# Kernel tuning notes

Hardware: AMD Instinct MI355X
Metric: run time of the kernel (lower is better)

The kernel has to match this reference:

```python
import jax, jax.numpy as jnp
import numpy as np

B, S, H = 8, 1024, 1024
NH, HD = 16, 64
EPS = 1e-12


def _p(w, g):
    # make_p_layer: w + gamma * clamp(w, min=0)
    return w + g * jnp.clip(w, 0.0, None)


def _pproc(x, W, b, g):
    # z = layer(x); zp = player(x); return zp * (z/zp).detach()  (value == z)
    z = x @ W.T + b
    zp = x @ _p(W, g).T + _p(b, g)
    return zp * jax.lax.stop_gradient(z / zp)


def _ln_nowb_detach(x):
    # 'nowb' LayerNorm (no weight/bias), mean and std detached (LNargsDetach)
    m = jax.lax.stop_gradient(jnp.mean(x, axis=-1, keepdims=True))
    v = jax.lax.stop_gradient(jnp.var(x, axis=-1, keepdims=True))
    return (x - m) / jnp.sqrt(v + EPS)


def setup_inputs() -> dict:
    key = jax.random.key(0)
    ks = jax.random.split(key, 10)
    lin = lambda k: (jax.random.normal(k, (H, H), jnp.float32) * 0.02)
    vec = lambda k: (jax.random.normal(k, (H,), jnp.float32) * 0.02)
    return {
        "hidden_states": jax.random.normal(ks[0], (B, S, H), jnp.float32),
        "Wq": lin(ks[1]), "bq": vec(ks[2]),
        "Wk": lin(ks[3]), "bk": vec(ks[4]),
        "Wv": lin(ks[5]), "bv": vec(ks[6]),
        "Wo": lin(ks[7]), "bo": vec(ks[8]),
        "gamma_AH": jnp.float32(0.1),
        "gamma_LN": jnp.float32(0.1),
    }


def reference(hidden_states, Wq, bq, Wk, bk, Wv, bv, Wo, bo, gamma_AH, gamma_LN):
    g = gamma_AH
    # dual-pass Q/K/V (pproc: value == plain linear, grads via perturbed layer)
    q = _pproc(hidden_states, Wq, bq, g)   # [B,S,H]
    k = _pproc(hidden_states, Wk, bk, g)
    v = _pproc(hidden_states, Wv, bv, g)
    split = lambda x: x.reshape(B, S, NH, HD).transpose(0, 2, 1, 3)  # [B,NH,S,HD]
    qt, kt, vt = split(q), split(k), split(v)
    # NOTE: original code does NOT scale by 1/sqrt(head_dim)
    scores = jnp.einsum('bhqd,bhkd->bhqk', qt, kt)
    attn = jax.nn.softmax(scores, axis=-1)
    probs = (1.0 - g) * jax.lax.stop_gradient(attn) + g * attn
    ctx = jnp.einsum('bhqk,bhkd->bhqd', probs, vt)
    ctx = ctx.transpose(0, 2, 1, 3).reshape(B, S, H)  # [B,S,H]
    # BertSelfOutput.pforward: perturbed dense (gamma_LN) + residual + detached LN
    h = ctx @ _p(Wo, gamma_LN).T + _p(bo, gamma_LN)
    out = _ln_nowb_detach(h + hidden_states)
    return out, probs
```

## Files before the change

kernel.cpp:

```cpp
#include <hip/hip_runtime.h>

typedef short short8 __attribute__((ext_vector_type(8)));
typedef float floatx4 __attribute__((ext_vector_type(4)));
typedef unsigned short ushort8v __attribute__((ext_vector_type(8)));

#define B_ 8
#define S_ 1024
#define H_ 1024
#define NH_ 16
#define HD_ 64

__device__ __forceinline__ unsigned short f2bf(float f) {
  unsigned u = __float_as_uint(f);
  u += 0x7fffu + ((u >> 16) & 1u);
  return (unsigned short)(u >> 16);
}

__device__ __forceinline__ floatx4 mfma16(short8 a, short8 b, floatx4 c) {
  return __builtin_amdgcn_mfma_f32_16x16x32_bf16(a, b, c, 0, 0, 0);
}

__global__ void __launch_bounds__(256) cvt_kernel(const float* __restrict__ src,
                                                  unsigned short* __restrict__ dst,
                                                  const float* __restrict__ gamma,
                                                  int n) {
  int i = (blockIdx.x * 256 + threadIdx.x) * 4;
  if (i >= n) return;
  float g = gamma ? gamma[0] : 0.0f;
  float4 v = *(const float4*)(src + i);
  ushort4 o;
  o.x = f2bf(v.x + g * fmaxf(v.x, 0.f));
  o.y = f2bf(v.y + g * fmaxf(v.y, 0.f));
  o.z = f2bf(v.z + g * fmaxf(v.z, 0.f));
  o.w = f2bf(v.w + g * fmaxf(v.w, 0.f));
  *(ushort4*)(dst + i) = o;
}

__device__ __forceinline__ void gemm_mainloop(const unsigned short* __restrict__ Ag,
                                              const unsigned short* __restrict__ Bg,
                                              int K,
                                              unsigned short* As, unsigned short* Bs,
                                              floatx4 acc[4][4]) {
  const int tid = threadIdx.x;
  const int l = tid & 63, w = tid >> 6;
  const int l15 = l & 15, l4 = l >> 4;
  const int wm = (w & 1) << 6, wn = (w >> 1) << 6;
  const int r0 = tid >> 2;
  const int c0 = (tid & 3) << 3;
  for (int k0 = 0; k0 < K; k0 += 32) {
    __syncthreads();
    *(uint4*)&As[r0 * 32 + c0]        = *(const uint4*)&Ag[(size_t)r0 * K + k0 + c0];
    *(uint4*)&As[(r0 + 64) * 32 + c0] = *(const uint4*)&Ag[(size_t)(r0 + 64) * K + k0 + c0];
    *(uint4*)&Bs[r0 * 32 + c0]        = *(const uint4*)&Bg[(size_t)r0 * K + k0 + c0];
    *(uint4*)&Bs[(r0 + 64) * 32 + c0] = *(const uint4*)&Bg[(size_t)(r0 + 64) * K + k0 + c0];
    __syncthreads();
    short8 a[4], bb[4];
#pragma unroll
    for (int i = 0; i < 4; ++i)
      a[i] = *(const short8*)&As[(wm + i * 16 + l15) * 32 + l4 * 8];
#pragma unroll
    for (int j = 0; j < 4; ++j)
      bb[j] = *(const short8*)&Bs[(wn + j * 16 + l15) * 32 + l4 * 8];
#pragma unroll
    for (int i = 0; i < 4; ++i)
#pragma unroll
      for (int j = 0; j < 4; ++j)
        acc[i][j] = mfma16(a[i], bb[j], acc[i][j]);
  }
}

__global__ void __launch_bounds__(256) gemm_qkv(
    const unsigned short* __restrict__ xb,
    const unsigned short* __restrict__ wq, const unsigned short* __restrict__ wk,
    const unsigned short* __restrict__ wv,
    const float* __restrict__ bq, const float* __restrict__ bk, const float* __restrict__ bv,
    unsigned short* __restrict__ oq, unsigned short* __restrict__ ok,
    unsigned short* __restrict__ ov) {
  __shared__ unsigned short As[128 * 32];
  __shared__ unsigned short Bs[128 * 32];
  const int z = blockIdx.z;
  const unsigned short* W = (z == 0) ? wq : (z == 1) ? wk : wv;
  const float* bias        = (z == 0) ? bq : (z == 1) ? bk : bv;
  unsigned short* O        = (z == 0) ? oq : (z == 1) ? ok : ov;
  const int nBase = blockIdx.x * 128, mBase = blockIdx.y * 128;
  floatx4 acc[4][4];
  const floatx4 fz = {0.f, 0.f, 0.f, 0.f};
#pragma unroll
  for (int i = 0; i < 4; ++i)
#pragma unroll
    for (int j = 0; j < 4; ++j) acc[i][j] = fz;
  gemm_mainloop(xb + (size_t)mBase * H_, W + (size_t)nBase * H_, H_, As, Bs, acc);
  const int l = threadIdx.x & 63, w = threadIdx.x >> 6;
  const int l15 = l & 15, l4 = l >> 4;
  const int wm = (w & 1) << 6, wn = (w >> 1) << 6;
#pragma unroll
  for (int i = 0; i < 4; ++i) {
    int row = mBase + wm + i * 16 + l4 * 4;
#pragma unroll
    for (int j = 0; j < 4; ++j) {
      int col = nBase + wn + j * 16 + l15;
      float bcol = bias[col];
#pragma unroll
      for (int r = 0; r < 4; ++r)
        O[(size_t)(row + r) * H_ + col] = f2bf(acc[i][j][r] + bcol);
    }
  }
}

__global__ void __launch_bounds__(256) transpose_v(const unsigned short* __restrict__ vb,
                                                   unsigned short* __restrict__ vt) {
  const int st = blockIdx.x, h = blockIdx.y, b = blockIdx.z;
  __shared__ unsigned short t[64 * 72];
  const int tid = threadIdx.x;
  const unsigned short* src = vb + (size_t)(b * S_ + st * 64) * H_ + h * HD_;
  for (int c = tid; c < 512; c += 256) {
    int i = c >> 3, dg = (c & 7) << 3;
    *(uint4*)&t[i * 72 + dg] = *(const uint4*)&src[(size_t)i * H_ + dg];
  }
  __syncthreads();
  unsigned short* dst = vt + ((size_t)(b * NH_ + h) * HD_) * S_ + st * 64;
  for (int c = tid; c < 512; c += 256) {
    int d = c >> 3, ig = (c & 7) << 3;
    ushort8v v;
#pragma unroll
    for (int ii = 0; ii < 8; ++ii) v[ii] = t[(ig + ii) * 72 + d];
    *(ushort8v*)&dst[(size_t)d * S_ + ig] = v;
  }
}

__global__ void __launch_bounds__(256) attn_kernel(
    const unsigned short* __restrict__ qg_, const unsigned short* __restrict__ kg_,
    const unsigned short* __restrict__ vtg_,
    float* __restrict__ probs, unsigned short* __restrict__ ctxb) {
  const int qt = blockIdx.x, h = blockIdx.y, b = blockIdx.z;
  __shared__ unsigned short Qs[64 * 64];
  __shared__ unsigned short Ks[128 * 64];
  __shared__ unsigned short Vts[64 * 128];
  __shared__ unsigned short Ps[64 * 128];
  const int tid = threadIdx.x;
  const int l = tid & 63, w = tid >> 6;
  const int l15 = l & 15, l4 = l >> 4;

  const unsigned short* qg = qg_ + ((size_t)(b * S_) + qt * 64) * H_ + h * HD_;
  const unsigned short* kg = kg_ + (size_t)(b * S_) * H_ + h * HD_;
  const unsigned short* vg = vtg_ + ((size_t)(b * NH_ + h) * HD_) * S_;

  for (int c = tid; c < 512; c += 256) {
    int row = c >> 3, cg = (c & 7) << 3;
    *(uint4*)&Qs[row * 64 + cg] = *(const uint4*)&qg[(size_t)row * H_ + cg];
  }
  __syncthreads();
  short8 aq0 = *(const short8*)&Qs[(w * 16 + l15) * 64 + l4 * 8];
  short8 aq1 = *(const short8*)&Qs[(w * 16 + l15) * 64 + 32 + l4 * 8];

  float esum[4] = {0.f, 0.f, 0.f, 0.f};
  for (int kt = 0; kt < 8; ++kt) {
    __syncthreads();
    for (int c = tid; c < 1024; c += 256) {
      int row = c >> 3, cg = (c & 7) << 3;
      *(uint4*)&Ks[row * 64 + cg] = *(const uint4*)&kg[(size_t)(kt * 128 + row) * H_ + cg];
    }
    __syncthreads();
#pragma unroll
    for (int j = 0; j < 8; ++j) {
      short8 b0 = *(const short8*)&Ks[(j * 16 + l15) * 64 + l4 * 8];
      short8 b1 = *(const short8*)&Ks[(j * 16 + l15) * 64 + 32 + l4 * 8];
      floatx4 s = {0.f, 0.f, 0.f, 0.f};
      s = mfma16(aq0, b0, s);
      s = mfma16(aq1, b1, s);
#pragma unroll
      for (int r = 0; r < 4; ++r) esum[r] += __expf(s[r]);
    }
  }
#pragma unroll
  for (int m = 1; m < 16; m <<= 1)
#pragma unroll
    for (int r = 0; r < 4; ++r) esum[r] += __shfl_xor(esum[r], m, 64);
  float rinv[4];
#pragma unroll
  for (int r = 0; r < 4; ++r) rinv[r] = 1.0f / esum[r];

  const floatx4 fz = {0.f, 0.f, 0.f, 0.f};
  floatx4 cacc[4];
#pragma unroll
  for (int dt = 0; dt < 4; ++dt) cacc[dt] = fz;
  const int qrow_base = qt * 64 + w * 16 + l4 * 4;
  for (int kt = 0; kt < 8; ++kt) {
    __syncthreads();
    for (int c = tid; c < 1024; c += 256) {
      int row = c >> 3, cg = (c & 7) << 3;
      *(uint4*)&Ks[row * 64 + cg] = *(const uint4*)&kg[(size_t)(kt * 128 + row) * H_ + cg];
    }
    for (int c = tid; c < 1024; c += 256) {
      int row = c >> 4, cg = (c & 15) << 3;
      *(uint4*)&Vts[row * 128 + cg] = *(const uint4*)&vg[(size_t)row * S_ + kt * 128 + cg];
    }
    __syncthreads();
#pragma unroll
    for (int j = 0; j < 8; ++j) {
      short8 b0 = *(const short8*)&Ks[(j * 16 + l15) * 64 + l4 * 8];
      short8 b1 = *(const short8*)&Ks[(j * 16 + l15) * 64 + 32 + l4 * 8];
      floatx4 s = {0.f, 0.f, 0.f, 0.f};
      s = mfma16(aq0, b0, s);
      s = mfma16(aq1, b1, s);
      float* pp = probs + ((size_t)((b * NH_ + h) * S_) + qrow_base) * S_ + kt * 128 + j * 16 + l15;
#pragma unroll
      for (int r = 0; r < 4; ++r) {
        float p = __expf(s[r]) * rinv[r];
        pp[(size_t)r * S_] = p;
        Ps[(w * 16 + l4 * 4 + r) * 128 + j * 16 + l15] = f2bf(p);
      }
    }
    __syncthreads();
    short8 ap[4];
#pragma unroll
    for (int ks = 0; ks < 4; ++ks)
      ap[ks] = *(const short8*)&Ps[(w * 16 + l15) * 128 + ks * 32 + l4 * 8];
#pragma unroll
    for (int dt = 0; dt < 4; ++dt)
#pragma unroll
      for (int ks = 0; ks < 4; ++ks) {
        short8 bv = *(const short8*)&Vts[(dt * 16 + l15) * 128 + ks * 32 + l4 * 8];
        cacc[dt] = mfma16(ap[ks], bv, cacc[dt]);
      }
  }
  const int rowg = b * S_ + qt * 64 + w * 16 + l4 * 4;
#pragma unroll
  for (int dt = 0; dt < 4; ++dt)
#pragma unroll
    for (int r = 0; r < 4; ++r)
      ctxb[(size_t)(rowg + r) * H_ + h * HD_ + dt * 16 + l15] = f2bf(cacc[dt][r]);
}

__global__ void __launch_bounds__(256) gemm_out(
    const unsigned short* __restrict__ ctxb, const unsigned short* __restrict__ wob,
    const float* __restrict__ bo, const float* __restrict__ gln,
    const float* __restrict__ xres, float* __restrict__ hres) {
  __shared__ unsigned short As[128 * 32];
  __shared__ unsigned short Bs[128 * 32];
  const int nBase = blockIdx.x * 128, mBase = blockIdx.y * 128;
  floatx4 acc[4][4];
  const floatx4 fz = {0.f, 0.f, 0.f, 0.f};
#pragma unroll
  for (int i = 0; i < 4; ++i)
#pragma unroll
    for (int j = 0; j < 4; ++j) acc[i][j] = fz;
  gemm_mainloop(ctxb + (size_t)mBase * H_, wob + (size_t)nBase * H_, H_, As, Bs, acc);
  const float g = gln[0];
  const int l = threadIdx.x & 63, w = threadIdx.x >> 6;
  const int l15 = l & 15, l4 = l >> 4;
  const int wm = (w & 1) << 6, wn = (w >> 1) << 6;
#pragma unroll
  for (int i = 0; i < 4; ++i) {
    int row = mBase + wm + i * 16 + l4 * 4;
#pragma unroll
    for (int j = 0; j < 4; ++j) {
      int col = nBase + wn + j * 16 + l15;
      float pb = bo[col];
      pb += g * fmaxf(pb, 0.f);
#pragma unroll
      for (int r = 0; r < 4; ++r)
        hres[(size_t)(row + r) * H_ + col] =
            acc[i][j][r] + pb + xres[(size_t)(row + r) * H_ + col];
    }
  }
}

__global__ void __launch_bounds__(256) ln_kernel(const float* __restrict__ hres,
                                                 float* __restrict__ out) {
  const int row = blockIdx.x;
  const int tid = threadIdx.x;
  const float* xr = hres + (size_t)row * H_;
  float4 v = *(const float4*)&xr[tid * 4];
  float s = v.x + v.y + v.z + v.w;
  float q = v.x * v.x + v.y * v.y + v.z * v.z + v.w * v.w;
#pragma unroll
  for (int m = 1; m < 64; m <<= 1) {
    s += __shfl_xor(s, m, 64);
    q += __shfl_xor(q, m, 64);
  }
  __shared__ float sh[8];
  const int w = tid >> 6, l = tid & 63;
  if (l == 0) { sh[w] = s; sh[4 + w] = q; }
  __syncthreads();
  s = sh[0] + sh[1] + sh[2] + sh[3];
  q = sh[4] + sh[5] + sh[6] + sh[7];
  float mean = s * (1.f / 1024.f);
  float var = q * (1.f / 1024.f) - mean * mean;
  float inv = rsqrtf(var + 1e-12f);
  float4 o;
  o.x = (v.x - mean) * inv;
  o.y = (v.y - mean) * inv;
  o.z = (v.z - mean) * inv;
  o.w = (v.w - mean) * inv;
  *(float4*)&out[(size_t)row * H_ + tid * 4] = o;
}

extern "C" void kernel_launch(void* const* d_in, const int* in_sizes, int n_in,
                              void* d_out, int out_size, void* d_ws, size_t ws_size,
                              hipStream_t stream) {
  const float* x   = (const float*)d_in[0];
  const float* Wq  = (const float*)d_in[1];
  const float* bq  = (const float*)d_in[2];
  const float* Wk  = (const float*)d_in[3];
  const float* bk  = (const float*)d_in[4];
  const float* Wv  = (const float*)d_in[5];
  const float* bv  = (const float*)d_in[6];
  const float* Wo  = (const float*)d_in[7];
  const float* bo  = (const float*)d_in[8];
  const float* gLN = (const float*)d_in[10];

  float* out   = (float*)d_out;
  float* probs = out + (size_t)B_ * S_ * H_;

  unsigned short* xb  = (unsigned short*)d_ws;
  unsigned short* wqb = xb + 8388608;
  unsigned short* wkb = wqb + 1048576;
  unsigned short* wvb = wkb + 1048576;
  unsigned short* wob = wvb + 1048576;
  unsigned short* qb  = wob + 1048576;
  unsigned short* kb  = qb + 8388608;
  unsigned short* vb  = kb + 8388608;
  unsigned short* vt  = vb + 8388608;
  unsigned short* ctxb = xb;
  float* hres = (float*)qb;

  cvt_kernel<<<8192, 256, 0, stream>>>(x, xb, nullptr, 8388608);
  cvt_kernel<<<1024, 256, 0, stream>>>(Wq, wqb, nullptr, 1048576);
  cvt_kernel<<<1024, 256, 0, stream>>>(Wk, wkb, nullptr, 1048576);
  cvt_kernel<<<1024, 256, 0, stream>>>(Wv, wvb, nullptr, 1048576);
  cvt_kernel<<<1024, 256, 0, stream>>>(Wo, wob, gLN, 1048576);

  gemm_qkv<<<dim3(8, 64, 3), 256, 0, stream>>>(xb, wqb, wkb, wvb, bq, bk, bv, qb, kb, vb);
  transpose_v<<<dim3(16, 16, 8), 256, 0, stream>>>(vb, vt);
  attn_kernel<<<dim3(16, 16, 8), 256, 0, stream>>>(qb, kb, vt, probs, ctxb);
  gemm_out<<<dim3(8, 64, 1), 256, 0, stream>>>(ctxb, wob, bo, gLN, x, hres);
  ln_kernel<<<8192, 256, 0, stream>>>(hres, out);
}
```

Before: 971.9 us.

## Use direct global-to-LDS loads with XOR-swizzled LDS layouts and merge weight converts

Replaces register-staged global->LDS copies in the GEMM mainloop and attention kernel with global_load_lds 16-byte direct loads. In attention, K, V^T and P tiles use an XOR swizzle so MFMA operand reads avoid LDS bank conflicts. The four weight conversion launches are merged into one kernel. This aims to cut VGPR traffic, bank conflicts and launch overhead, but it relies on the lane-to-address mapping that global_load_lds requires and adds index arithmetic.

```diff
diff --git a/kernel.cpp b/kernel.cpp
--- a/kernel.cpp
+++ b/kernel.cpp
@@ -20,13 +20,32 @@
   return __builtin_amdgcn_mfma_f32_16x16x32_bf16(a, b, c, 0, 0, 0);
 }
 
-__global__ void __launch_bounds__(256) cvt_kernel(const float* __restrict__ src,
-                                                  unsigned short* __restrict__ dst,
-                                                  const float* __restrict__ gamma,
-                                                  int n) {
+__device__ __forceinline__ void gload16(const void* g, void* lds) {
+  __builtin_amdgcn_global_load_lds(
+      (const __attribute__((address_space(1))) unsigned int*)g,
+      (__attribute__((address_space(3))) unsigned int*)lds, 16, 0, 0);
+}
+
+__global__ void __launch_bounds__(256) cvt_x(const float* __restrict__ src,
+                                             unsigned short* __restrict__ dst) {
   int i = (blockIdx.x * 256 + threadIdx.x) * 4;
-  if (i >= n) return;
-  float g = gamma ? gamma[0] : 0.0f;
+  float4 v = *(const float4*)(src + i);
+  ushort4 o;
+  o.x = f2bf(v.x); o.y = f2bf(v.y); o.z = f2bf(v.z); o.w = f2bf(v.w);
+  *(ushort4*)(dst + i) = o;
+}
+
+__global__ void __launch_bounds__(256) cvt_w(
+    const float* __restrict__ W0, const float* __restrict__ W1,
+    const float* __restrict__ W2, const float* __restrict__ W3,
+    unsigned short* __restrict__ o0, unsigned short* __restrict__ o1,
+    unsigned short* __restrict__ o2, unsigned short* __restrict__ o3,
+    const float* __restrict__ gLN) {
+  const int which = blockIdx.y;
+  const float* src = (which == 0) ? W0 : (which == 1) ? W1 : (which == 2) ? W2 : W3;
+  unsigned short* dst = (which == 0) ? o0 : (which == 1) ? o1 : (which == 2) ? o2 : o3;
+  const float g = (which == 3) ? gLN[0] : 0.0f;
+  int i = (blockIdx.x * 256 + threadIdx.x) * 4;
   float4 v = *(const float4*)(src + i);
   ushort4 o;
   o.x = f2bf(v.x + g * fmaxf(v.x, 0.f));
@@ -45,14 +64,14 @@
   const int l = tid & 63, w = tid >> 6;
   const int l15 = l & 15, l4 = l >> 4;
   const int wm = (w & 1) << 6, wn = (w >> 1) << 6;
-  const int r0 = tid >> 2;
-  const int c0 = (tid & 3) << 3;
+  const int srow = w * 32 + (l >> 2);
+  const int scol = (l & 3) << 3;
   for (int k0 = 0; k0 < K; k0 += 32) {
     __syncthreads();
-    *(uint4*)&As[r0 * 32 + c0]        = *(const uint4*)&Ag[(size_t)r0 * K + k0 + c0];
-    *(uint4*)&As[(r0 + 64) * 32 + c0] = *(const uint4*)&Ag[(size_t)(r0 + 64) * K + k0 + c0];
-    *(uint4*)&Bs[r0 * 32 + c0]        = *(const uint4*)&Bg[(size_t)r0 * K + k0 + c0];
-    *(uint4*)&Bs[(r0 + 64) * 32 + c0] = *(const uint4*)&Bg[(size_t)(r0 + 64) * K + k0 + c0];
+    gload16(&Ag[(size_t)srow * K + k0 + scol],        &As[srow * 32 + scol]);
+    gload16(&Ag[(size_t)(srow + 16) * K + k0 + scol], &As[(srow + 16) * 32 + scol]);
+    gload16(&Bg[(size_t)srow * K + k0 + scol],        &Bs[srow * 32 + scol]);
+    gload16(&Bg[(size_t)(srow + 16) * K + k0 + scol], &Bs[(srow + 16) * 32 + scol]);
     __syncthreads();
     short8 a[4], bb[4];
 #pragma unroll
@@ -76,8 +95,8 @@
     const float* __restrict__ bq, const float* __restrict__ bk, const float* __restrict__ bv,
     unsigned short* __restrict__ oq, unsigned short* __restrict__ ok,
     unsigned short* __restrict__ ov) {
-  __shared__ unsigned short As[128 * 32];
-  __shared__ unsigned short Bs[128 * 32];
+  __shared__ __align__(16) unsigned short As[128 * 32];
+  __shared__ __align__(16) unsigned short Bs[128 * 32];
   const int z = blockIdx.z;
   const unsigned short* W = (z == 0) ? wq : (z == 1) ? wk : wv;
   const float* bias        = (z == 0) ? bq : (z == 1) ? bk : bv;
@@ -110,7 +129,7 @@
 __global__ void __launch_bounds__(256) transpose_v(const unsigned short* __restrict__ vb,
                                                    unsigned short* __restrict__ vt) {
   const int st = blockIdx.x, h = blockIdx.y, b = blockIdx.z;
-  __shared__ unsigned short t[64 * 72];
+  __shared__ __align__(16) unsigned short t[64 * 72];
   const int tid = threadIdx.x;
   const unsigned short* src = vb + (size_t)(b * S_ + st * 64) * H_ + h * HD_;
   for (int c = tid; c < 512; c += 256) {
@@ -133,21 +152,25 @@
     const unsigned short* __restrict__ vtg_,
     float* __restrict__ probs, unsigned short* __restrict__ ctxb) {
   const int qt = blockIdx.x, h = blockIdx.y, b = blockIdx.z;
-  __shared__ unsigned short Qs[64 * 64];
-  __shared__ unsigned short Ks[128 * 64];
-  __shared__ unsigned short Vts[64 * 128];
-  __shared__ unsigned short Ps[64 * 128];
+  __shared__ __align__(16) unsigned short Qs[64 * 64];
+  __shared__ __align__(16) unsigned short Ks[128 * 64];
+  __shared__ __align__(16) unsigned short Vts[64 * 128];
+  __shared__ __align__(16) unsigned short Ps[64 * 128];
   const int tid = threadIdx.x;
   const int l = tid & 63, w = tid >> 6;
   const int l15 = l & 15, l4 = l >> 4;
+  const int l7 = l & 7, lr8 = l >> 3;
 
   const unsigned short* qg = qg_ + ((size_t)(b * S_) + qt * 64) * H_ + h * HD_;
   const unsigned short* kg = kg_ + (size_t)(b * S_) * H_ + h * HD_;
   const unsigned short* vg = vtg_ + ((size_t)(b * NH_ + h) * HD_) * S_;
 
-  for (int c = tid; c < 512; c += 256) {
-    int row = c >> 3, cg = (c & 7) << 3;
-    *(uint4*)&Qs[row * 64 + cg] = *(const uint4*)&qg[(size_t)row * H_ + cg];
+  const int kcol = (l7 ^ lr8) << 3;
+
+#pragma unroll
+  for (int c = 0; c < 2; ++c) {
+    int row = w * 16 + c * 8 + lr8;
+    gload16(&qg[(size_t)row * H_ + (l7 << 3)], &Qs[row * 64 + (l7 << 3)]);
   }
   __syncthreads();
   short8 aq0 = *(const short8*)&Qs[(w * 16 + l15) * 64 + l4 * 8];
@@ -156,15 +179,17 @@
   float esum[4] = {0.f, 0.f, 0.f, 0.f};
   for (int kt = 0; kt < 8; ++kt) {
     __syncthreads();
-    for (int c = tid; c < 1024; c += 256) {
-      int row = c >> 3, cg = (c & 7) << 3;
-      *(uint4*)&Ks[row * 64 + cg] = *(const uint4*)&kg[(size_t)(kt * 128 + row) * H_ + cg];
+#pragma unroll
+    for (int c = 0; c < 4; ++c) {
+      int row = w * 32 + c * 8 + lr8;
+      gload16(&kg[(size_t)(kt * 128 + row) * H_ + kcol], &Ks[row * 64 + (l7 << 3)]);
     }
     __syncthreads();
 #pragma unroll
     for (int j = 0; j < 8; ++j) {
-      short8 b0 = *(const short8*)&Ks[(j * 16 + l15) * 64 + l4 * 8];
-      short8 b1 = *(const short8*)&Ks[(j * 16 + l15) * 64 + 32 + l4 * 8];
+      int rr = l15 & 7;
+      short8 b0 = *(const short8*)&Ks[(j * 16 + l15) * 64 + ((l4 ^ rr) << 3)];
+      short8 b1 = *(const short8*)&Ks[(j * 16 + l15) * 64 + (((4 + l4) ^ rr) << 3)];
       floatx4 s = {0.f, 0.f, 0.f, 0.f};
       s = mfma16(aq0, b0, s);
       s = mfma16(aq1, b1, s);
@@ -187,19 +212,23 @@
   const int qrow_base = qt * 64 + w * 16 + l4 * 4;
   for (int kt = 0; kt < 8; ++kt) {
     __syncthreads();
-    for (int c = tid; c < 1024; c += 256) {
-      int row = c >> 3, cg = (c & 7) << 3;
-      *(uint4*)&Ks[row * 64 + cg] = *(const uint4*)&kg[(size_t)(kt * 128 + row) * H_ + cg];
-    }
-    for (int c = tid; c < 1024; c += 256) {
-      int row = c >> 4, cg = (c & 15) << 3;
-      *(uint4*)&Vts[row * 128 + cg] = *(const uint4*)&vg[(size_t)row * S_ + kt * 128 + cg];
+#pragma unroll
+    for (int c = 0; c < 4; ++c) {
+      int row = w * 32 + c * 8 + lr8;
+      gload16(&kg[(size_t)(kt * 128 + row) * H_ + kcol], &Ks[row * 64 + (l7 << 3)]);
+    }
+#pragma unroll
+    for (int c = 0; c < 4; ++c) {
+      int row = w * 16 + c * 4 + l4;
+      int scol = (l15 ^ (c * 4 + l4)) << 3;
+      gload16(&vg[(size_t)row * S_ + kt * 128 + scol], &Vts[row * 128 + (l15 << 3)]);
     }
     __syncthreads();
 #pragma unroll
     for (int j = 0; j < 8; ++j) {
-      short8 b0 = *(const short8*)&Ks[(j * 16 + l15) * 64 + l4 * 8];
-      short8 b1 = *(const short8*)&Ks[(j * 16 + l15) * 64 + 32 + l4 * 8];
+      int rr = l15 & 7;
+      short8 b0 = *(const short8*)&Ks[(j * 16 + l15) * 64 + ((l4 ^ rr) << 3)];
+      short8 b1 = *(const short8*)&Ks[(j * 16 + l15) * 64 + (((4 + l4) ^ rr) << 3)];
       floatx4 s = {0.f, 0.f, 0.f, 0.f};
       s = mfma16(aq0, b0, s);
       s = mfma16(aq1, b1, s);
@@ -208,19 +237,21 @@
       for (int r = 0; r < 4; ++r) {
         float p = __expf(s[r]) * rinv[r];
         pp[(size_t)r * S_] = p;
-        Ps[(w * 16 + l4 * 4 + r) * 128 + j * 16 + l15] = f2bf(p);
+        int prow = w * 16 + l4 * 4 + r;
+        int pslot = (j * 2 + (l15 >> 3)) ^ (l4 * 4 + r);
+        Ps[prow * 128 + (pslot << 3) + (l15 & 7)] = f2bf(p);
       }
     }
     __syncthreads();
     short8 ap[4];
 #pragma unroll
     for (int ks = 0; ks < 4; ++ks)
-      ap[ks] = *(const short8*)&Ps[(w * 16 + l15) * 128 + ks * 32 + l4 * 8];
+      ap[ks] = *(const short8*)&Ps[(w * 16 + l15) * 128 + (((ks * 4 + l4) ^ l15) << 3)];
 #pragma unroll
     for (int dt = 0; dt < 4; ++dt)
 #pragma unroll
       for (int ks = 0; ks < 4; ++ks) {
-        short8 bv = *(const short8*)&Vts[(dt * 16 + l15) * 128 + ks * 32 + l4 * 8];
+        short8 bv = *(const short8*)&Vts[(dt * 16 + l15) * 128 + (((ks * 4 + l4) ^ l15) << 3)];
         cacc[dt] = mfma16(ap[ks], bv, cacc[dt]);
       }
   }
@@ -236,8 +267,8 @@
     const unsigned short* __restrict__ ctxb, const unsigned short* __restrict__ wob,
     const float* __restrict__ bo, const float* __restrict__ gln,
     const float* __restrict__ xres, float* __restrict__ hres) {
-  __shared__ unsigned short As[128 * 32];
-  __shared__ unsigned short Bs[128 * 32];
+  __shared__ __align__(16) unsigned short As[128 * 32];
+  __shared__ __align__(16) unsigned short Bs[128 * 32];
   const int nBase = blockIdx.x * 128, mBase = blockIdx.y * 128;
   floatx4 acc[4][4];
   const floatx4 fz = {0.f, 0.f, 0.f, 0.f};
@@ -325,11 +356,8 @@
   unsigned short* ctxb = xb;
   float* hres = (float*)qb;
 
-  cvt_kernel<<<8192, 256, 0, stream>>>(x, xb, nullptr, 8388608);
-  cvt_kernel<<<1024, 256, 0, stream>>>(Wq, wqb, nullptr, 1048576);
-  cvt_kernel<<<1024, 256, 0, stream>>>(Wk, wkb, nullptr, 1048576);
-  cvt_kernel<<<1024, 256, 0, stream>>>(Wv, wvb, nullptr, 1048576);
-  cvt_kernel<<<1024, 256, 0, stream>>>(Wo, wob, gLN, 1048576);
+  cvt_x<<<8192, 256, 0, stream>>>(x, xb);
+  cvt_w<<<dim3(1024, 4), 256, 0, stream>>>(Wq, Wk, Wv, Wo, wqb, wkb, wvb, wob, gLN);
 
   gemm_qkv<<<dim3(8, 64, 3), 256, 0, stream>>>(xb, wqb, wkb, wvb, bq, bk, bv, qb, kb, vb);
   transpose_v<<<dim3(16, 16, 8), 256, 0, stream>>>(vb, vt);
```

Result: faster. 827.0 us (-14.9%).
